# Kernel optimization log

Hardware: AMD Instinct MI355X
Metric: run time of the kernel (lower is better)

## Reference

```python
import jax, jax.numpy as jnp
import numpy as np

B, S, LC, DIM, H, FFN = 1, 3600, 512, 1536, 12, 8960
HD = DIM // H          # 128
GRID = (4, 30, 30)     # f*h*w == S
K_LEN = 9900           # hardcoded k_lens in SelfAttention.forward
EPS = 1e-6

def _rope_axis_angles(n_pos, dim):
    inv = 1.0 / np.power(10000.0, np.arange(0, dim, 2, dtype=np.float64) / dim)
    return np.outer(np.arange(n_pos), inv)

def _build_rope(grid, head_dim):
    c = head_dim // 2                      # 64
    c1, c2 = c - 2 * (c // 3), c // 3      # 22, 21 (Wan 3D rope split)
    f, h, w = grid
    af = _rope_axis_angles(f, 2 * c1)
    ah = _rope_axis_angles(h, 2 * c2)
    aw = _rope_axis_angles(w, 2 * c2)
    ang = np.concatenate([
        np.broadcast_to(af[:, None, None, :], (f, h, w, c1)),
        np.broadcast_to(ah[None, :, None, :], (f, h, w, c2)),
        np.broadcast_to(aw[None, None, :, :], (f, h, w, c2)),
    ], axis=-1).reshape(f * h * w, c)
    return np.cos(ang).astype(np.float32), np.sin(ang).astype(np.float32)

def setup_inputs():
    key = jax.random.key(0)
    ks = iter(jax.random.split(key, 40))
    cos, sin = _build_rope(GRID, HD)
    inp = {
        'x': jax.random.normal(next(ks), (B, S, DIM), dtype=jnp.float32),
        'context': jax.random.normal(next(ks), (B, LC, DIM), dtype=jnp.float32),
        't_mod': 0.1 * jax.random.normal(next(ks), (B, 6, DIM), dtype=jnp.float32),
        'rope_cos': jnp.asarray(cos), 'rope_sin': jnp.asarray(sin),
        'modulation': jax.random.normal(next(ks), (1, 6, DIM), dtype=jnp.float32) / DIM ** 0.5,
    }
    for p in ('sa', 'ca'):
        for w in ('q', 'k', 'v', 'o'):
            inp[p + '_' + w + 'w'] = 0.02 * jax.random.normal(next(ks), (DIM, DIM), dtype=jnp.float32)
            inp[p + '_' + w + 'b'] = jnp.zeros((DIM,), jnp.float32)
        inp[p + '_nq'] = jnp.ones((DIM,), jnp.float32)
        inp[p + '_nk'] = jnp.ones((DIM,), jnp.float32)
    inp['n3_w'] = jnp.ones((DIM,), jnp.float32)
    inp['n3_b'] = jnp.zeros((DIM,), jnp.float32)
    inp['ffn_w1'] = 0.02 * jax.random.normal(next(ks), (DIM, FFN), dtype=jnp.float32)
    inp['ffn_b1'] = jnp.zeros((FFN,), jnp.float32)
    inp['ffn_w2'] = 0.02 * jax.random.normal(next(ks), (FFN, DIM), dtype=jnp.float32)
    inp['ffn_b2'] = jnp.zeros((DIM,), jnp.float32)
    return inp

def _rms(x, w):
    x32 = x.astype(jnp.float32)
    n = x32 * jax.lax.rsqrt(jnp.mean(x32 * x32, axis=-1, keepdims=True) + EPS)
    return n.astype(x.dtype) * w

def _ln(x, w=None, b=None):
    mu = jnp.mean(x, axis=-1, keepdims=True)
    var = jnp.mean(jnp.square(x - mu), axis=-1, keepdims=True)
    y = (x - mu) * jax.lax.rsqrt(var + EPS)
    return y if w is None else y * w + b

def _rope(x, cos, sin):
    b, s, h, d = x.shape
    x2 = x.reshape(b, s, h, d // 2, 2)
    xe, xo = x2[..., 0], x2[..., 1]
    c, sn = cos[None, :, None, :], sin[None, :, None, :]
    return jnp.stack([xe * c - xo * sn, xe * sn + xo * c], axis=-1).reshape(b, s, h, d)

def _attn(q, k, v, k_len=None):
    # q,k,v: [B,S,H,D]
    scores = jnp.einsum('bqhd,bkhd->bhqk', q, k) * (q.shape[-1] ** -0.5)
    if k_len is not None:
        mask = jnp.arange(k.shape[1]) < k_len
        scores = jnp.where(mask[None, None, None, :], scores, jnp.finfo(scores.dtype).min)
    return jnp.einsum('bhqk,bkhd->bqhd', jax.nn.softmax(scores, axis=-1), v)

def reference(x, context, t_mod, rope_cos, rope_sin, modulation,
              sa_qw, sa_qb, sa_kw, sa_kb, sa_vw, sa_vb, sa_ow, sa_ob, sa_nq, sa_nk,
              ca_qw, ca_qb, ca_kw, ca_kb, ca_vw, ca_vb, ca_ow, ca_ob, ca_nq, ca_nk,
              n3_w, n3_b, ffn_w1, ffn_b1, ffn_w2, ffn_b2):
    mod = modulation + t_mod                      # [B,6,DIM]
    sh_msa, sc_msa, g_msa, sh_mlp, sc_mlp, g_mlp = [mod[:, i:i + 1] for i in range(6)]
    b = x.shape[0]
    # --- self-attention with AdaLN modulate + 3D RoPE + k_lens mask ---
    h = _ln(x) * (1 + sc_msa) + sh_msa
    q = _rms(h @ sa_qw + sa_qb, sa_nq).reshape(b, -1, H, HD)
    k = _rms(h @ sa_kw + sa_kb, sa_nk).reshape(b, -1, H, HD)
    v = (h @ sa_vw + sa_vb).reshape(b, -1, H, HD)
    a = _attn(_rope(q, rope_cos, rope_sin), _rope(k, rope_cos, rope_sin), v, k_len=K_LEN)
    x = x + g_msa * (a.reshape(b, -1, DIM) @ sa_ow + sa_ob)
    # --- cross-attention ---
    hc = _ln(x, n3_w, n3_b)
    q = _rms(hc @ ca_qw + ca_qb, ca_nq).reshape(b, -1, H, HD)
    k = _rms(context @ ca_kw + ca_kb, ca_nk).reshape(b, -1, H, HD)
    v = (context @ ca_vw + ca_vb).reshape(b, -1, H, HD)
    x = x + (_attn(q, k, v).reshape(b, -1, DIM) @ ca_ow + ca_ob)
    # --- gated FFN with AdaLN modulate ---
    h = _ln(x) * (1 + sc_mlp) + sh_mlp
    h = jax.nn.gelu(h @ ffn_w1 + ffn_b1, approximate=True) @ ffn_w2 + ffn_b2
    return x + g_mlp * h
```

## Files before the change

kernel.cpp:

```cpp
#include <hip/hip_runtime.h>
#include <cstdint>

#define S_LEN 3600
#define DMODEL 1536
#define LCTX 512
#define NH 12
#define HDIM 128
#define FFND 8960
#define SPAD_SELF 3648

typedef short v8s __attribute__((ext_vector_type(8)));
typedef float v4f __attribute__((ext_vector_type(4)));
typedef unsigned short u16b;
typedef unsigned int u32b;

#define AS1 __attribute__((address_space(1)))
#define AS3 __attribute__((address_space(3)))

__device__ __forceinline__ void gl_lds16(const void* g, void* l){
  __builtin_amdgcn_global_load_lds((AS1 const void*)g, (AS3 void*)l, 16, 0, 0);
}

__device__ __forceinline__ u16b f2b(float f){
  union { float f; u32b i; } x; x.f = f;
  u32b r = x.i + 0x7fffu + ((x.i >> 16) & 1u);
  return (u16b)(r >> 16);
}

__device__ __forceinline__ int swz4(int row){ return (row ^ (row >> 2)) & 3; }

__global__ void add_vec(const float* __restrict__ a, const float* __restrict__ b,
                        float* __restrict__ o, int n){
  int i = blockIdx.x * 256 + threadIdx.x;
  if (i < n) o[i] = a[i] + b[i];
}

__global__ void f2b_kernel(const float* __restrict__ in, u16b* __restrict__ out, int n){
  int i = blockIdx.x * 256 + threadIdx.x;
  if (i < n) out[i] = f2b(in[i]);
}

struct WJob { const float* W; u16b* WT; int K; int N; int t0; };
struct WJobs { WJob j[10]; };

__global__ __launch_bounds__(256) void wconv(WJobs jobs){
  __shared__ float tile[32][33];
  int b = blockIdx.x;
  int ji = 0;
  #pragma unroll
  for (int i = 0; i < 10; ++i) if (b >= jobs.j[i].t0) ji = i;
  WJob jb = jobs.j[ji];
  int rel = b - jb.t0;
  int ntn = jb.N / 32;
  int k0 = (rel / ntn) * 32, n0 = (rel % ntn) * 32;
  int tx = threadIdx.x & 31, ty = threadIdx.x >> 5;
  #pragma unroll
  for (int r = ty; r < 32; r += 8) tile[r][tx] = jb.W[(size_t)(k0 + r) * jb.N + n0 + tx];
  __syncthreads();
  #pragma unroll
  for (int r = ty; r < 32; r += 8) jb.WT[(size_t)(n0 + r) * jb.K + k0 + tx] = f2b(tile[tx][r]);
}

__global__ __launch_bounds__(256) void vtrans(const u16b* __restrict__ V,
                                              u16b* __restrict__ Vt,
                                              int S, int Spad){
  __shared__ u16b t[32][136];
  int h = blockIdx.y, kb = blockIdx.x * 32, tid = threadIdx.x;
  int row = tid >> 3, ch = tid & 7;
  int key = kb + row;
  if (key < S){
    float4 a = *(const float4*)(V + (size_t)key * DMODEL + h * HDIM + ch * 16);
    float4 b = *(const float4*)(V + (size_t)key * DMODEL + h * HDIM + ch * 16 + 8);
    *(float4*)&t[row][ch * 16] = a;
    *(float4*)&t[row][ch * 16 + 8] = b;
  } else {
    float4 z = {0.f, 0.f, 0.f, 0.f};
    *(float4*)&t[row][ch * 16] = z;
    *(float4*)&t[row][ch * 16 + 8] = z;
  }
  __syncthreads();
  int hd = tid >> 1, kc = (tid & 1) * 16;
  u16b* dst = Vt + ((size_t)h * HDIM + hd) * Spad + kb + kc;
  #pragma unroll
  for (int e = 0; e < 16; e += 2){
    u32b pk = ((u32b)t[kc + e][hd]) | (((u32b)t[kc + e + 1][hd]) << 16);
    *(u32b*)(dst + e) = pk;
  }
}

__global__ __launch_bounds__(256) void ln_mod(const float* __restrict__ X,
                                              const float* __restrict__ gamma,
                                              const float* __restrict__ beta,
                                              float gadd, u16b* __restrict__ out){
  int row = blockIdx.x;
  const float* xr = X + (size_t)row * DMODEL;
  int tid = threadIdx.x;
  float v[6]; float s1 = 0.f, s2 = 0.f;
  #pragma unroll
  for (int j = 0; j < 6; ++j){ v[j] = xr[tid + j * 256]; s1 += v[j]; s2 += v[j] * v[j]; }
  #pragma unroll
  for (int o = 1; o < 64; o <<= 1){ s1 += __shfl_xor(s1, o); s2 += __shfl_xor(s2, o); }
  __shared__ float red[8];
  int wid = tid >> 6, lane = tid & 63;
  if (!lane){ red[wid * 2] = s1; red[wid * 2 + 1] = s2; }
  __syncthreads();
  s1 = red[0] + red[2] + red[4] + red[6];
  s2 = red[1] + red[3] + red[5] + red[7];
  float mu = s1 / DMODEL;
  float var = s2 / DMODEL - mu * mu;
  float rstd = rsqrtf(var + 1e-6f);
  #pragma unroll
  for (int j = 0; j < 6; ++j){
    int c = tid + j * 256;
    float g = gamma[c] + gadd;
    float b = beta[c];
    out[(size_t)row * DMODEL + c] = f2b((v[j] - mu) * rstd * g + b);
  }
}

__global__ __launch_bounds__(256) void rms_rope(const float* __restrict__ X,
                                                const float* __restrict__ w,
                                                const float* __restrict__ cosT,
                                                const float* __restrict__ sinT,
                                                u16b* __restrict__ out){
  int row = blockIdx.x;
  const float* xr = X + (size_t)row * DMODEL;
  int tid = threadIdx.x;
  float2 v[3]; float ss = 0.f;
  #pragma unroll
  for (int j = 0; j < 3; ++j){
    v[j] = *(const float2*)(xr + 2 * (tid + j * 256));
    ss += v[j].x * v[j].x + v[j].y * v[j].y;
  }
  #pragma unroll
  for (int o = 1; o < 64; o <<= 1) ss += __shfl_xor(ss, o);
  __shared__ float red[4];
  int wid = tid >> 6, lane = tid & 63;
  if (!lane) red[wid] = ss;
  __syncthreads();
  ss = red[0] + red[1] + red[2] + red[3];
  float rstd = rsqrtf(ss / DMODEL + 1e-6f);
  #pragma unroll
  for (int j = 0; j < 3; ++j){
    int p = tid + j * 256;
    float xe = v[j].x * rstd * w[2 * p];
    float xo = v[j].y * rstd * w[2 * p + 1];
    float oe, oo;
    if (cosT){
      int d = p & 63;
      float c = cosT[row * 64 + d], sn = sinT[row * 64 + d];
      oe = xe * c - xo * sn; oo = xe * sn + xo * c;
    } else { oe = xe; oo = xo; }
    u32b packed = ((u32b)f2b(oe)) | (((u32b)f2b(oo)) << 16);
    *(u32b*)(out + (size_t)row * DMODEL + 2 * p) = packed;
  }
}

template<int EPI>
__global__ __launch_bounds__(256, 2) void gemm_bt(
    const u16b* __restrict__ A, const u16b* __restrict__ BT,
    const float* __restrict__ bias, const float* __restrict__ res,
    const float* __restrict__ gate, float* __restrict__ outF,
    u16b* __restrict__ outB, int M, int N, int K, int kLen)
{
  __shared__ char Asm[2][8192];
  __shared__ char Bsm[2][8192];
  const int tid = threadIdx.x, lane = tid & 63, wid = tid >> 6;
  const int bm = blockIdx.x * 128, bn = blockIdx.y * 128;
  const int kbase = blockIdx.z * kLen;
  const int wm = (wid >> 1) * 64, wn = (wid & 1) * 64;
  v4f acc[4][4] = {};

  auto stage = [&](int buf, int k0){
    #pragma unroll
    for (int c = 0; c < 2; ++c){
      int seg = wid * 2 + c;
      int l = seg * 64 + lane;
      int row = l >> 2, cs = l & 3;
      int col = cs ^ swz4(row);
      gl_lds16(A + (size_t)min(bm + row, M - 1) * K + kbase + k0 + col * 8,
               Asm[buf] + seg * 1024);
      gl_lds16(BT + (size_t)(bn + row) * K + kbase + k0 + col * 8,
               Bsm[buf] + seg * 1024);
    }
  };

  const int nt = kLen / 32;
  int cur = 0;
  stage(0, 0);
  __syncthreads();
  const int chk = lane >> 4, qr = lane & 15;
  for (int t = 0; t < nt; ++t){
    if (t + 1 < nt) stage(cur ^ 1, (t + 1) * 32);
    char* Ab = Asm[cur]; char* Bb = Bsm[cur];
    v8s af[4], bfr[4];
    #pragma unroll
    for (int f = 0; f < 4; ++f){
      int rowa = wm + f * 16 + qr;
      af[f] = *(const v8s*)(Ab + rowa * 64 + ((chk ^ swz4(rowa)) * 16));
      int rowb = wn + f * 16 + qr;
      bfr[f] = *(const v8s*)(Bb + rowb * 64 + ((chk ^ swz4(rowb)) * 16));
    }
    __builtin_amdgcn_s_setprio(1);
    #pragma unroll
    for (int i = 0; i < 4; ++i)
      #pragma unroll
      for (int j = 0; j < 4; ++j)
        acc[i][j] = __builtin_amdgcn_mfma_f32_16x16x32_bf16(af[i], bfr[j], acc[i][j], 0, 0, 0);
    __builtin_amdgcn_s_setprio(0);
    __syncthreads();
    cur ^= 1;
  }
  const int rr = lane >> 4;
  #pragma unroll
  for (int i = 0; i < 4; ++i){
    #pragma unroll
    for (int j = 0; j < 4; ++j){
      int n = bn + wn + j * 16 + qr;
      float bv = (EPI != 5 && bias) ? bias[n] : 0.f;
      float gv = (EPI == 2 && gate) ? gate[n] : 1.f;
      #pragma unroll
      for (int r = 0; r < 4; ++r){
        int m = bm + wm + i * 16 + rr * 4 + r;
        if (m < M){
          float val = acc[i][j][r] + bv;
          size_t idx = (size_t)m * N + n;
          if (EPI == 0) outB[idx] = f2b(val);
          else if (EPI == 1) outF[idx] = val;
          else if (EPI == 2) outF[idx] = res[idx] + gv * val;
          else if (EPI == 5) outF[(size_t)blockIdx.z * M * N + idx] = val;
          else {
            float t3 = val * val * val;
            float th = tanhf(0.7978845608028654f * (val + 0.044715f * t3));
            outB[idx] = f2b(0.5f * val * (1.f + th));
          }
        }
      }
    }
  }
}

struct Seg { const float* bias; float* outF; u16b* outB; };
struct Segs { Seg s[3]; };

__global__ __launch_bounds__(256, 2) void gemm_seg(
    const u16b* __restrict__ A, const u16b* __restrict__ BT,
    Segs segs, int M, int N, int K)
{
  __shared__ char Asm[2][8192];
  __shared__ char Bsm[2][8192];
  const int tid = threadIdx.x, lane = tid & 63, wid = tid >> 6;
  const int bm = blockIdx.x * 128, bn = blockIdx.y * 128;
  const int wm = (wid >> 1) * 64, wn = (wid & 1) * 64;
  v4f acc[4][4] = {};

  auto stage = [&](int buf, int k0){
    #pragma unroll
    for (int c = 0; c < 2; ++c){
      int seg = wid * 2 + c;
      int l = seg * 64 + lane;
      int row = l >> 2, cs = l & 3;
      int col = cs ^ swz4(row);
      gl_lds16(A + (size_t)min(bm + row, M - 1) * K + k0 + col * 8,
               Asm[buf] + seg * 1024);
      gl_lds16(BT + (size_t)(bn + row) * K + k0 + col * 8,
               Bsm[buf] + seg * 1024);
    }
  };

  const int nt = K / 32;
  int cur = 0;
  stage(0, 0);
  __syncthreads();
  const int chk = lane >> 4, qr = lane & 15;
  for (int t = 0; t < nt; ++t){
    if (t + 1 < nt) stage(cur ^ 1, (t + 1) * 32);
    char* Ab = Asm[cur]; char* Bb = Bsm[cur];
    v8s af[4], bfr[4];
    #pragma unroll
    for (int f = 0; f < 4; ++f){
      int rowa = wm + f * 16 + qr;
      af[f] = *(const v8s*)(Ab + rowa * 64 + ((chk ^ swz4(rowa)) * 16));
      int rowb = wn + f * 16 + qr;
      bfr[f] = *(const v8s*)(Bb + rowb * 64 + ((chk ^ swz4(rowb)) * 16));
    }
    __builtin_amdgcn_s_setprio(1);
    #pragma unroll
    for (int i = 0; i < 4; ++i)
      #pragma unroll
      for (int j = 0; j < 4; ++j)
        acc[i][j] = __builtin_amdgcn_mfma_f32_16x16x32_bf16(af[i], bfr[j], acc[i][j], 0, 0, 0);
    __builtin_amdgcn_s_setprio(0);
    __syncthreads();
    cur ^= 1;
  }
  const int seg = bn / 1536;
  const Seg sg = segs.s[seg];
  const int rr = lane >> 4;
  #pragma unroll
  for (int i = 0; i < 4; ++i){
    #pragma unroll
    for (int j = 0; j < 4; ++j){
      int nloc = bn - seg * 1536 + wn + j * 16 + qr;
      float bv = sg.bias[nloc];
      #pragma unroll
      for (int r = 0; r < 4; ++r){
        int m = bm + wm + i * 16 + rr * 4 + r;
        if (m < M){
          float val = acc[i][j][r] + bv;
          size_t idx = (size_t)m * 1536 + nloc;
          if (sg.outB) sg.outB[idx] = f2b(val);
          else sg.outF[idx] = val;
        }
      }
    }
  }
}

__global__ __launch_bounds__(256) void ffn2_reduce(const float* __restrict__ part,
                                                   const float* __restrict__ res,
                                                   const float* __restrict__ bias,
                                                   const float* __restrict__ gate,
                                                   float* __restrict__ out, int total){
  int i4 = blockIdx.x * 256 + threadIdx.x;
  if (i4 * 4 >= total) return;
  int base = i4 * 4;
  int n = base % DMODEL;
  float4 p0 = *(const float4*)(part + base);
  float4 p1 = *(const float4*)(part + (size_t)total + base);
  float4 rs = *(const float4*)(res + base);
  float4 bv = *(const float4*)(bias + n);
  float4 gv = *(const float4*)(gate + n);
  float4 o;
  o.x = rs.x + gv.x * (p0.x + p1.x + bv.x);
  o.y = rs.y + gv.y * (p0.y + p1.y + bv.y);
  o.z = rs.z + gv.z * (p0.z + p1.z + bv.z);
  o.w = rs.w + gv.w * (p0.w + p1.w + bv.w);
  *(float4*)(out + base) = o;
}

__global__ __launch_bounds__(256, 2) void flash_attn(
    const u16b* __restrict__ Q, const u16b* __restrict__ Kp,
    const u16b* __restrict__ Vt, u16b* __restrict__ O,
    int Sq, int Sk, int Spad)
{
  __shared__ char KV[2][32768];
  __shared__ char Pall[8192];
  const int tid = threadIdx.x, lane = tid & 63, wid = tid >> 6;
  const int h = blockIdx.y;
  const int q0 = blockIdx.x * 64 + wid * 16;
  const int qq = lane & 15, cc = lane >> 4;
  char* Pb = Pall + wid * 2048;

  v8s qf[4];
  {
    int qrow = min(q0 + qq, Sq - 1);
    const u16b* qp = Q + (size_t)qrow * DMODEL + h * HDIM + cc * 8;
    #pragma unroll
    for (int ks = 0; ks < 4; ++ks) qf[ks] = *(const v8s*)(qp + ks * 32);
  }

  auto stage = [&](int buf, int kb0){
    char* base = KV[buf];
    #pragma unroll
    for (int c = 0; c < 4; ++c){
      int seg = wid * 4 + c;
      int g = seg * 64 + lane;
      int krow = g >> 4, kcol = (g & 15) ^ (krow & 7);
      gl_lds16(Kp + (size_t)min(kb0 + krow, Sk - 1) * DMODEL + h * HDIM + kcol * 8,
               base + seg * 1024);
      int vrow = g >> 3, vcol = (g & 7) ^ (vrow & 7);
      gl_lds16(Vt + ((size_t)h * HDIM + vrow) * Spad + kb0 + vcol * 8,
               base + 16384 + seg * 1024);
    }
  };

  float mrun = -1e30f, lrun = 0.f;
  v4f oacc[8] = {};
  const float scale = 0.08838834764831845f;
  const int nt = (Sk + 63) >> 6;
  int cur = 0;
  stage(0, 0);
  __syncthreads();

  for (int t = 0; t < nt; ++t){
    if (t + 1 < nt) stage(cur ^ 1, (t + 1) << 6);
    char* Kb = KV[cur]; char* Vb = KV[cur] + 16384;
    int kb0 = t << 6;
    v4f sc[4];
    __builtin_amdgcn_s_setprio(1);
    #pragma unroll
    for (int sub = 0; sub < 4; ++sub){
      v4f sa = {0.f, 0.f, 0.f, 0.f};
      int row = sub * 16 + qq;
      #pragma unroll
      for (int ks = 0; ks < 4; ++ks){
        v8s kf = *(const v8s*)(Kb + row * 256 + (((ks * 4 + cc) ^ (row & 7)) * 16));
        sa = __builtin_amdgcn_mfma_f32_16x16x32_bf16(kf, qf[ks], sa, 0, 0, 0);
      }
      sc[sub] = sa;
    }
    __builtin_amdgcn_s_setprio(0);
    #pragma unroll
    for (int sub = 0; sub < 4; ++sub)
      #pragma unroll
      for (int r = 0; r < 4; ++r) sc[sub][r] *= scale;
    if (kb0 + 64 > Sk){
      #pragma unroll
      for (int sub = 0; sub < 4; ++sub)
        #pragma unroll
        for (int r = 0; r < 4; ++r)
          if (kb0 + sub * 16 + cc * 4 + r >= Sk) sc[sub][r] = -1e30f;
    }
    float pmax = sc[0][0];
    #pragma unroll
    for (int sub = 0; sub < 4; ++sub)
      #pragma unroll
      for (int r = 0; r < 4; ++r) pmax = fmaxf(pmax, sc[sub][r]);
    pmax = fmaxf(pmax, __shfl_xor(pmax, 16));
    pmax = fmaxf(pmax, __shfl_xor(pmax, 32));
    if (!__all(pmax <= mrun + 8.f)){
      float mnew = fmaxf(mrun, pmax);
      float alpha = __expf(mrun - mnew);
      mrun = mnew;
      float alr[4];
      #pragma unroll
      for (int r = 0; r < 4; ++r) alr[r] = __shfl(alpha, cc * 4 + r);
      #pragma unroll
      for (int f = 0; f < 8; ++f)
        #pragma unroll
        for (int r = 0; r < 4; ++r) oacc[f][r] *= alr[r];
      lrun *= alpha;
    }
    float csum = 0.f;
    #pragma unroll
    for (int sub = 0; sub < 4; ++sub)
      #pragma unroll
      for (int r = 0; r < 4; ++r){
        float p = __expf(sc[sub][r] - mrun);
        sc[sub][r] = p; csum += p;
      }
    csum += __shfl_xor(csum, 16);
    csum += __shfl_xor(csum, 32);
    lrun += csum;
    #pragma unroll
    for (int sub = 0; sub < 4; ++sub){
      u32b u01 = ((u32b)f2b(sc[sub][0])) | (((u32b)f2b(sc[sub][1])) << 16);
      u32b u23 = ((u32b)f2b(sc[sub][2])) | (((u32b)f2b(sc[sub][3])) << 16);
      int gI = sub * 2 + (cc >> 1);
      uint2 w2; w2.x = u01; w2.y = u23;
      *(uint2*)(Pb + qq * 128 + ((gI ^ (qq & 7)) * 16) + (cc & 1) * 8) = w2;
    }
    v8s pf0 = *(const v8s*)(Pb + qq * 128 + (((cc) ^ (qq & 7)) * 16));
    v8s pf1 = *(const v8s*)(Pb + qq * 128 + (((4 + cc) ^ (qq & 7)) * 16));
    __builtin_amdgcn_s_setprio(1);
    #pragma unroll
    for (int hdb = 0; hdb < 8; ++hdb){
      int row = hdb * 16 + qq;
      v8s vf0 = *(const v8s*)(Vb + row * 128 + (((cc) ^ (row & 7)) * 16));
      v8s vf1 = *(const v8s*)(Vb + row * 128 + (((4 + cc) ^ (row & 7)) * 16));
      oacc[hdb] = __builtin_amdgcn_mfma_f32_16x16x32_bf16(pf0, vf0, oacc[hdb], 0, 0, 0);
      oacc[hdb] = __builtin_amdgcn_mfma_f32_16x16x32_bf16(pf1, vf1, oacc[hdb], 0, 0, 0);
    }
    __builtin_amdgcn_s_setprio(0);
    __syncthreads();
    cur ^= 1;
  }

  float linv = 1.f / lrun;
  float lr[4];
  #pragma unroll
  for (int r = 0; r < 4; ++r) lr[r] = __shfl(linv, cc * 4 + r);
  #pragma unroll
  for (int hdb = 0; hdb < 8; ++hdb)
    #pragma unroll
    for (int r = 0; r < 4; ++r){
      int qrow = q0 + cc * 4 + r;
      if (qrow < Sq)
        O[(size_t)qrow * DMODEL + h * HDIM + hdb * 16 + qq] = f2b(oacc[hdb][r] * lr[r]);
    }
}

extern "C" void kernel_launch(void* const* d_in, const int* in_sizes, int n_in,
                              void* d_out, int out_size, void* d_ws, size_t ws_size,
                              hipStream_t stream){
  (void)in_sizes; (void)n_in; (void)out_size; (void)ws_size;
  const float* x     = (const float*)d_in[0];
  const float* ctx   = (const float*)d_in[1];
  const float* t_mod = (const float*)d_in[2];
  const float* ropec = (const float*)d_in[3];
  const float* ropes = (const float*)d_in[4];
  const float* modu  = (const float*)d_in[5];
  const float* sa_qw = (const float*)d_in[6];  const float* sa_qb = (const float*)d_in[7];
  const float* sa_kw = (const float*)d_in[8];  const float* sa_kb = (const float*)d_in[9];
  const float* sa_vw = (const float*)d_in[10]; const float* sa_vb = (const float*)d_in[11];
  const float* sa_ow = (const float*)d_in[12]; const float* sa_ob = (const float*)d_in[13];
  const float* sa_nq = (const float*)d_in[14]; const float* sa_nk = (const float*)d_in[15];
  const float* ca_qw = (const float*)d_in[16]; const float* ca_qb = (const float*)d_in[17];
  const float* ca_kw = (const float*)d_in[18]; const float* ca_kb = (const float*)d_in[19];
  const float* ca_vw = (const float*)d_in[20]; const float* ca_vb = (const float*)d_in[21];
  const float* ca_ow = (const float*)d_in[22]; const float* ca_ob = (const float*)d_in[23];
  const float* ca_nq = (const float*)d_in[24]; const float* ca_nk = (const float*)d_in[25];
  const float* n3w   = (const float*)d_in[26]; const float* n3b   = (const float*)d_in[27];
  const float* fw1   = (const float*)d_in[28]; const float* fb1   = (const float*)d_in[29];
  const float* fw2   = (const float*)d_in[30]; const float* fb2   = (const float*)d_in[31];
  float* out = (float*)d_out;

  char* wsp = (char*)d_ws;
  size_t off = 0;
  auto alloc = [&](size_t b){ void* p = wsp + off; off += (b + 255) & ~(size_t)255; return p; };
  const size_t WW = (size_t)DMODEL * DMODEL * 2;
  float* modc = (float*)alloc(6 * DMODEL * 4);
  u16b* w1T   = (u16b*)alloc((size_t)FFND * DMODEL * 2);
  u16b* w2T   = (u16b*)alloc((size_t)DMODEL * FFND * 2);
  u16b* h_bf  = (u16b*)alloc((size_t)S_LEN * DMODEL * 2);
  float* pre0 = (float*)alloc((size_t)S_LEN * DMODEL * 4);
  size_t region0 = off;
  u16b* sa_qkvT = (u16b*)alloc(3 * WW);
  u16b* sa_owT  = (u16b*)alloc(WW);
  u16b* ca_qwT  = (u16b*)alloc(WW);
  u16b* ca_kvT  = (u16b*)alloc(2 * WW);
  u16b* ca_owT  = (u16b*)alloc(WW);
  float* x2    = (float*)alloc((size_t)S_LEN * DMODEL * 4);
  float* pre2  = (float*)alloc((size_t)LCTX * DMODEL * 4);
  u16b* qb     = (u16b*)alloc((size_t)S_LEN * DMODEL * 2);
  u16b* kb     = (u16b*)alloc((size_t)S_LEN * DMODEL * 2);
  u16b* vb     = (u16b*)alloc((size_t)S_LEN * DMODEL * 2);
  u16b* ab     = (u16b*)alloc((size_t)S_LEN * DMODEL * 2);
  u16b* ctxb   = (u16b*)alloc((size_t)LCTX * DMODEL * 2);
  u16b* k2b    = (u16b*)alloc((size_t)LCTX * DMODEL * 2);
  u16b* v2b    = (u16b*)alloc((size_t)LCTX * DMODEL * 2);
  u16b* vts    = (u16b*)alloc((size_t)NH * HDIM * SPAD_SELF * 2);
  u16b* vtc    = (u16b*)alloc((size_t)NH * HDIM * LCTX * 2);
  u16b* fmid = (u16b*)(wsp + region0);
  float* fpart = (float*)(wsp + region0 + (size_t)S_LEN * FFND * 2);

  add_vec<<<36, 256, 0, stream>>>(modu, t_mod, modc, 6 * DMODEL);

  WJobs jobs; int t = 0;
  auto addjob = [&](int i, const float* w_, u16b* wt, int K, int N){
    jobs.j[i].W = w_; jobs.j[i].WT = wt; jobs.j[i].K = K; jobs.j[i].N = N; jobs.j[i].t0 = t;
    t += (K / 32) * (N / 32);
  };
  addjob(0, sa_qw, sa_qkvT, DMODEL, DMODEL);
  addjob(1, sa_kw, sa_qkvT + (size_t)DMODEL * DMODEL, DMODEL, DMODEL);
  addjob(2, sa_vw, sa_qkvT + (size_t)2 * DMODEL * DMODEL, DMODEL, DMODEL);
  addjob(3, sa_ow, sa_owT, DMODEL, DMODEL);
  addjob(4, ca_qw, ca_qwT, DMODEL, DMODEL);
  addjob(5, ca_kw, ca_kvT, DMODEL, DMODEL);
  addjob(6, ca_vw, ca_kvT + (size_t)DMODEL * DMODEL, DMODEL, DMODEL);
  addjob(7, ca_ow, ca_owT, DMODEL, DMODEL);
  addjob(8, fw1, w1T, DMODEL, FFND);
  addjob(9, fw2, w2T, FFND, DMODEL);
  wconv<<<t, 256, 0, stream>>>(jobs);

  f2b_kernel<<<(LCTX * DMODEL) / 256, 256, 0, stream>>>(ctx, ctxb, LCTX * DMODEL);

  ln_mod<<<S_LEN, 256, 0, stream>>>(x, modc + DMODEL, modc, 1.f, h_bf);
  dim3 g12(29, 12);
  {
    Segs sg;
    sg.s[0] = { sa_qb, pre0, nullptr };
    sg.s[1] = { sa_kb, x2,   nullptr };
    sg.s[2] = { sa_vb, nullptr, vb   };
    gemm_seg<<<dim3(29, 36), 256, 0, stream>>>(h_bf, sa_qkvT, sg, S_LEN, 3 * DMODEL, DMODEL);
  }
  rms_rope<<<S_LEN, 256, 0, stream>>>(pre0, sa_nq, ropec, ropes, qb);
  rms_rope<<<S_LEN, 256, 0, stream>>>(x2, sa_nk, ropec, ropes, kb);
  vtrans<<<dim3(SPAD_SELF / 32, 12), 256, 0, stream>>>(vb, vts, S_LEN, SPAD_SELF);
  flash_attn<<<dim3(57, 12), 256, 0, stream>>>(qb, kb, vts, ab, S_LEN, S_LEN, SPAD_SELF);
  gemm_bt<2><<<g12, 256, 0, stream>>>(ab, sa_owT, sa_ob, x, modc + 2 * DMODEL, x2, nullptr, S_LEN, DMODEL, DMODEL, DMODEL);

  ln_mod<<<S_LEN, 256, 0, stream>>>(x2, n3w, n3b, 0.f, h_bf);
  gemm_bt<1><<<g12, 256, 0, stream>>>(h_bf, ca_qwT, ca_qb, nullptr, nullptr, pre0, nullptr, S_LEN, DMODEL, DMODEL, DMODEL);
  {
    Segs sg;
    sg.s[0] = { ca_kb, pre2, nullptr };
    sg.s[1] = { ca_vb, nullptr, v2b  };
    sg.s[2] = { ca_vb, nullptr, v2b  };
    gemm_seg<<<dim3(4, 24), 256, 0, stream>>>(ctxb, ca_kvT, sg, LCTX, 2 * DMODEL, DMODEL);
  }
  rms_rope<<<S_LEN, 256, 0, stream>>>(pre0, ca_nq, nullptr, nullptr, qb);
  rms_rope<<<LCTX, 256, 0, stream>>>(pre2, ca_nk, nullptr, nullptr, k2b);
  vtrans<<<dim3(16, 12), 256, 0, stream>>>(v2b, vtc, LCTX, LCTX);
  flash_attn<<<dim3(57, 12), 256, 0, stream>>>(qb, k2b, vtc, ab, S_LEN, LCTX, LCTX);
  gemm_bt<2><<<g12, 256, 0, stream>>>(ab, ca_owT, ca_ob, x2, nullptr, pre0, nullptr, S_LEN, DMODEL, DMODEL, DMODEL);

  ln_mod<<<S_LEN, 256, 0, stream>>>(pre0, modc + 4 * DMODEL, modc + 3 * DMODEL, 1.f, h_bf);
  gemm_bt<3><<<dim3(29, 70), 256, 0, stream>>>(h_bf, w1T, fb1, nullptr, nullptr, nullptr, fmid, S_LEN, FFND, DMODEL, DMODEL);
  gemm_bt<5><<<dim3(29, 12, 2), 256, 0, stream>>>(fmid, w2T, nullptr, nullptr, nullptr, fpart, nullptr, S_LEN, DMODEL, FFND, FFND / 2);
  ffn2_reduce<<<(S_LEN * DMODEL / 4 + 255) / 256, 256, 0, stream>>>(fpart, pre0, fb2, modc + 5 * DMODEL, out, S_LEN * DMODEL);
}
```

Before: 1.055 ms.

## Split attention over key range with a merge kernel and fold softmax scale into Q

Flash attention now splits the key range into two halves along a third grid dimension. Each half writes unnormalised fp32 partial outputs plus per-row (max, sum) to scratch buffers, and a new merge_o kernel combines them. The aim is more blocks and higher occupancy: the launch bound rises to 4 and the K/V staging drops from double to single buffering. The softmax scale times log2(e) is folded into Q inside rms_rope, so the kernel can use exp2 without a per-score multiply, and P is packed with a native bf16 pack instruction. The cost is an extra kernel, fp32 partial traffic, loss of load/compute overlap within a block, and reuse of existing workspace buffers as scratch; it is not clear the reused kb buffer is large enough to hold fp32 data.

```diff
diff --git a/kernel.cpp b/kernel.cpp
--- a/kernel.cpp
+++ b/kernel.cpp
@@ -25,6 +25,12 @@
   union { float f; u32b i; } x; x.f = f;
   u32b r = x.i + 0x7fffu + ((x.i >> 16) & 1u);
   return (u16b)(r >> 16);
+}
+
+__device__ __forceinline__ u32b cvtpk(float a, float b){
+  u32b r;
+  asm("v_cvt_pk_bf16_f32 %0, %1, %2" : "=v"(r) : "v"(a), "v"(b));
+  return r;
 }
 
 __device__ __forceinline__ int swz4(int row){ return (row ^ (row >> 2)) & 3; }
@@ -122,6 +128,7 @@
                                                 const float* __restrict__ w,
                                                 const float* __restrict__ cosT,
                                                 const float* __restrict__ sinT,
+                                                float qmul,
                                                 u16b* __restrict__ out){
   int row = blockIdx.x;
   const float* xr = X + (size_t)row * DMODEL;
@@ -151,6 +158,7 @@
       float c = cosT[row * 64 + d], sn = sinT[row * 64 + d];
       oe = xe * c - xo * sn; oo = xe * sn + xo * c;
     } else { oe = xe; oo = xo; }
+    oe *= qmul; oo *= qmul;
     u32b packed = ((u32b)f2b(oe)) | (((u32b)f2b(oo)) << 16);
     *(u32b*)(out + (size_t)row * DMODEL + 2 * p) = packed;
   }
@@ -339,17 +347,45 @@
   *(float4*)(out + base) = o;
 }
 
-__global__ __launch_bounds__(256, 2) void flash_attn(
+__global__ __launch_bounds__(256) void merge_o(const float* __restrict__ op0,
+                                               const float* __restrict__ op1,
+                                               const float2* __restrict__ ml,
+                                               u16b* __restrict__ outO, int Sq){
+  int i4 = blockIdx.x * 256 + threadIdx.x;
+  const int perRow = DMODEL / 4;
+  if (i4 >= Sq * perRow) return;
+  int row = i4 / perRow, c4 = (i4 % perRow) * 4;
+  int h = c4 >> 7;
+  float2 ml0 = ml[h * Sq + row];
+  float2 ml1 = ml[NH * Sq + h * Sq + row];
+  float M = fmaxf(ml0.x, ml1.x);
+  float w0 = exp2f(ml0.x - M), w1 = exp2f(ml1.x - M);
+  float inv = 1.f / (ml0.y * w0 + ml1.y * w1);
+  float4 a = *(const float4*)(op0 + (size_t)row * DMODEL + c4);
+  float4 b = *(const float4*)(op1 + (size_t)row * DMODEL + c4);
+  u32b lo = ((u32b)f2b((a.x * w0 + b.x * w1) * inv)) | (((u32b)f2b((a.y * w0 + b.y * w1) * inv)) << 16);
+  u32b hi = ((u32b)f2b((a.z * w0 + b.z * w1) * inv)) | (((u32b)f2b((a.w * w0 + b.w * w1) * inv)) << 16);
+  uint2 w2; w2.x = lo; w2.y = hi;
+  *(uint2*)(outO + (size_t)row * DMODEL + c4) = w2;
+}
+
+__global__ __launch_bounds__(256, 4) void flash_attn(
     const u16b* __restrict__ Q, const u16b* __restrict__ Kp,
     const u16b* __restrict__ Vt, u16b* __restrict__ O,
-    int Sq, int Sk, int Spad)
+    float* __restrict__ op0, float* __restrict__ op1,
+    float2* __restrict__ mlbuf,
+    int Sq, int Sk, int ksplit, int Spad)
 {
-  __shared__ char KV[2][32768];
+  __shared__ char KV[32768];
   __shared__ char Pall[8192];
   const int tid = threadIdx.x, lane = tid & 63, wid = tid >> 6;
   const int h = blockIdx.y;
+  const int z = blockIdx.z;
+  const int kbeg = z * ksplit;
+  const int kend = min(kbeg + ksplit, Sk);
   const int q0 = blockIdx.x * 64 + wid * 16;
   const int qq = lane & 15, cc = lane >> 4;
+  char* Kb = KV; char* Vb = KV + 16384;
   char* Pb = Pall + wid * 2048;
 
   v8s qf[4];
@@ -360,33 +396,28 @@
     for (int ks = 0; ks < 4; ++ks) qf[ks] = *(const v8s*)(qp + ks * 32);
   }
 
-  auto stage = [&](int buf, int kb0){
-    char* base = KV[buf];
+  auto stage = [&](int kb0){
     #pragma unroll
     for (int c = 0; c < 4; ++c){
       int seg = wid * 4 + c;
       int g = seg * 64 + lane;
       int krow = g >> 4, kcol = (g & 15) ^ (krow & 7);
       gl_lds16(Kp + (size_t)min(kb0 + krow, Sk - 1) * DMODEL + h * HDIM + kcol * 8,
-               base + seg * 1024);
+               Kb + seg * 1024);
       int vrow = g >> 3, vcol = (g & 7) ^ (vrow & 7);
       gl_lds16(Vt + ((size_t)h * HDIM + vrow) * Spad + kb0 + vcol * 8,
-               base + 16384 + seg * 1024);
+               Vb + seg * 1024);
     }
   };
 
   float mrun = -1e30f, lrun = 0.f;
   v4f oacc[8] = {};
-  const float scale = 0.08838834764831845f;
-  const int nt = (Sk + 63) >> 6;
-  int cur = 0;
-  stage(0, 0);
-  __syncthreads();
+  const int nt = (kend - kbeg + 63) >> 6;
 
   for (int t = 0; t < nt; ++t){
-    if (t + 1 < nt) stage(cur ^ 1, (t + 1) << 6);
-    char* Kb = KV[cur]; char* Vb = KV[cur] + 16384;
-    int kb0 = t << 6;
+    int kb0 = kbeg + (t << 6);
+    stage(kb0);
+    __syncthreads();
     v4f sc[4];
     __builtin_amdgcn_s_setprio(1);
     #pragma unroll
@@ -401,27 +432,23 @@
       sc[sub] = sa;
     }
     __builtin_amdgcn_s_setprio(0);
-    #pragma unroll
-    for (int sub = 0; sub < 4; ++sub)
-      #pragma unroll
-      for (int r = 0; r < 4; ++r) sc[sub][r] *= scale;
-    if (kb0 + 64 > Sk){
+    if (kb0 + 64 > kend){
       #pragma unroll
       for (int sub = 0; sub < 4; ++sub)
         #pragma unroll
         for (int r = 0; r < 4; ++r)
-          if (kb0 + sub * 16 + cc * 4 + r >= Sk) sc[sub][r] = -1e30f;
-    }
-    float pmax = sc[0][0];
-    #pragma unroll
-    for (int sub = 0; sub < 4; ++sub)
-      #pragma unroll
-      for (int r = 0; r < 4; ++r) pmax = fmaxf(pmax, sc[sub][r]);
+          if (kb0 + sub * 16 + cc * 4 + r >= kend) sc[sub][r] = -1e30f;
+    }
+    float m01 = fmaxf(fmaxf(sc[0][0], sc[0][1]), fmaxf(sc[0][2], sc[0][3]));
+    float m23 = fmaxf(fmaxf(sc[1][0], sc[1][1]), fmaxf(sc[1][2], sc[1][3]));
+    float m45 = fmaxf(fmaxf(sc[2][0], sc[2][1]), fmaxf(sc[2][2], sc[2][3]));
+    float m67 = fmaxf(fmaxf(sc[3][0], sc[3][1]), fmaxf(sc[3][2], sc[3][3]));
+    float pmax = fmaxf(fmaxf(m01, m23), fmaxf(m45, m67));
     pmax = fmaxf(pmax, __shfl_xor(pmax, 16));
     pmax = fmaxf(pmax, __shfl_xor(pmax, 32));
-    if (!__all(pmax <= mrun + 8.f)){
+    if (!__all(pmax <= mrun + 11.54f)){
       float mnew = fmaxf(mrun, pmax);
-      float alpha = __expf(mrun - mnew);
+      float alpha = exp2f(mrun - mnew);
       mrun = mnew;
       float alr[4];
       #pragma unroll
@@ -434,21 +461,26 @@
     }
     float csum = 0.f;
     #pragma unroll
-    for (int sub = 0; sub < 4; ++sub)
-      #pragma unroll
-      for (int r = 0; r < 4; ++r){
-        float p = __expf(sc[sub][r] - mrun);
-        sc[sub][r] = p; csum += p;
+    for (int sub = 0; sub < 4; ++sub){
+      float s0 = 0.f, s1 = 0.f;
+      #pragma unroll
+      for (int r = 0; r < 4; r += 2){
+        float p0 = exp2f(sc[sub][r] - mrun);
+        float p1 = exp2f(sc[sub][r + 1] - mrun);
+        sc[sub][r] = p0; sc[sub][r + 1] = p1;
+        s0 += p0; s1 += p1;
       }
+      csum += s0 + s1;
+    }
     csum += __shfl_xor(csum, 16);
     csum += __shfl_xor(csum, 32);
     lrun += csum;
     #pragma unroll
     for (int sub = 0; sub < 4; ++sub){
-      u32b u01 = ((u32b)f2b(sc[sub][0])) | (((u32b)f2b(sc[sub][1])) << 16);
-      u32b u23 = ((u32b)f2b(sc[sub][2])) | (((u32b)f2b(sc[sub][3])) << 16);
+      uint2 w2;
+      w2.x = cvtpk(sc[sub][0], sc[sub][1]);
+      w2.y = cvtpk(sc[sub][2], sc[sub][3]);
       int gI = sub * 2 + (cc >> 1);
-      uint2 w2; w2.x = u01; w2.y = u23;
       *(uint2*)(Pb + qq * 128 + ((gI ^ (qq & 7)) * 16) + (cc & 1) * 8) = w2;
     }
     v8s pf0 = *(const v8s*)(Pb + qq * 128 + (((cc) ^ (qq & 7)) * 16));
@@ -464,21 +496,34 @@
     }
     __builtin_amdgcn_s_setprio(0);
     __syncthreads();
-    cur ^= 1;
-  }
-
-  float linv = 1.f / lrun;
-  float lr[4];
-  #pragma unroll
-  for (int r = 0; r < 4; ++r) lr[r] = __shfl(linv, cc * 4 + r);
-  #pragma unroll
-  for (int hdb = 0; hdb < 8; ++hdb)
-    #pragma unroll
-    for (int r = 0; r < 4; ++r){
-      int qrow = q0 + cc * 4 + r;
-      if (qrow < Sq)
-        O[(size_t)qrow * DMODEL + h * HDIM + hdb * 16 + qq] = f2b(oacc[hdb][r] * lr[r]);
-    }
+  }
+
+  if (mlbuf){
+    float* op = z ? op1 : op0;
+    #pragma unroll
+    for (int hdb = 0; hdb < 8; ++hdb)
+      #pragma unroll
+      for (int r = 0; r < 4; ++r){
+        int qrow = q0 + cc * 4 + r;
+        if (qrow < Sq)
+          op[(size_t)qrow * DMODEL + h * HDIM + hdb * 16 + qq] = oacc[hdb][r];
+      }
+    if (cc == 0 && q0 + qq < Sq)
+      mlbuf[(size_t)z * NH * Sq + (size_t)h * Sq + q0 + qq] = make_float2(mrun, lrun);
+  } else {
+    float linv = 1.f / lrun;
+    float lr[4];
+    #pragma unroll
+    for (int r = 0; r < 4; ++r) lr[r] = __shfl(linv, cc * 4 + r);
+    #pragma unroll
+    for (int hdb = 0; hdb < 8; ++hdb)
+      #pragma unroll
+      for (int r = 0; r < 4; ++r){
+        int qrow = q0 + cc * 4 + r;
+        if (qrow < Sq)
+          O[(size_t)qrow * DMODEL + h * HDIM + hdb * 16 + qq] = f2b(oacc[hdb][r] * lr[r]);
+      }
+  }
 }
 
 extern "C" void kernel_launch(void* const* d_in, const int* in_sizes, int n_in,
@@ -505,6 +550,8 @@
   const float* fw1   = (const float*)d_in[28]; const float* fb1   = (const float*)d_in[29];
   const float* fw2   = (const float*)d_in[30]; const float* fb2   = (const float*)d_in[31];
   float* out = (float*)d_out;
+
+  const float QSCALE = 0.08838834764831845f * 1.4426950408889634f;
 
   char* wsp = (char*)d_ws;
   size_t off = 0;
@@ -565,10 +612,13 @@
     sg.s[2] = { sa_vb, nullptr, vb   };
     gemm_seg<<<dim3(29, 36), 256, 0, stream>>>(h_bf, sa_qkvT, sg, S_LEN, 3 * DMODEL, DMODEL);
   }
-  rms_rope<<<S_LEN, 256, 0, stream>>>(pre0, sa_nq, ropec, ropes, qb);
-  rms_rope<<<S_LEN, 256, 0, stream>>>(x2, sa_nk, ropec, ropes, kb);
+  rms_rope<<<S_LEN, 256, 0, stream>>>(pre0, sa_nq, ropec, ropes, QSCALE, qb);
+  rms_rope<<<S_LEN, 256, 0, stream>>>(x2, sa_nk, ropec, ropes, 1.f, kb);
   vtrans<<<dim3(SPAD_SELF / 32, 12), 256, 0, stream>>>(vb, vts, S_LEN, SPAD_SELF);
-  flash_attn<<<dim3(57, 12), 256, 0, stream>>>(qb, kb, vts, ab, S_LEN, S_LEN, SPAD_SELF);
+  flash_attn<<<dim3(57, 12, 2), 256, 0, stream>>>(qb, kb, vts, ab,
+      (float*)pre0, (float*)x2, (float2*)vb, S_LEN, S_LEN, 1856, SPAD_SELF);
+  merge_o<<<(S_LEN * (DMODEL / 4) + 255) / 256, 256, 0, stream>>>(
+      (const float*)pre0, (const float*)x2, (const float2*)vb, ab, S_LEN);
   gemm_bt<2><<<g12, 256, 0, stream>>>(ab, sa_owT, sa_ob, x, modc + 2 * DMODEL, x2, nullptr, S_LEN, DMODEL, DMODEL, DMODEL);
 
   ln_mod<<<S_LEN, 256, 0, stream>>>(x2, n3w, n3b, 0.f, h_bf);
@@ -580,10 +630,13 @@
     sg.s[2] = { ca_vb, nullptr, v2b  };
     gemm_seg<<<dim3(4, 24), 256, 0, stream>>>(ctxb, ca_kvT, sg, LCTX, 2 * DMODEL, DMODEL);
   }
-  rms_rope<<<S_LEN, 256, 0, stream>>>(pre0, ca_nq, nullptr, nullptr, qb);
-  rms_rope<<<LCTX, 256, 0, stream>>>(pre2, ca_nk, nullptr, nullptr, k2b);
+  rms_rope<<<S_LEN, 256, 0, stream>>>(pre0, ca_nq, nullptr, nullptr, QSCALE, qb);
+  rms_rope<<<LCTX, 256, 0, stream>>>(pre2, ca_nk, nullptr, nullptr, 1.f, k2b);
   vtrans<<<dim3(16, 12), 256, 0, stream>>>(v2b, vtc, LCTX, LCTX);
-  flash_attn<<<dim3(57, 12), 256, 0, stream>>>(qb, k2b, vtc, ab, S_LEN, LCTX, LCTX);
+  flash_attn<<<dim3(57, 12, 2), 256, 0, stream>>>(qb, k2b, vtc, ab,
+      (float*)pre0, (float*)kb, (float2*)vts, S_LEN, LCTX, 256, LCTX);
+  merge_o<<<(S_LEN * (DMODEL / 4) + 255) / 256, 256, 0, stream>>>(
+      (const float*)pre0, (const float*)kb, (const float2*)vts, ab, S_LEN);
   gemm_bt<2><<<g12, 256, 0, stream>>>(ab, ca_owT, ca_ob, x2, nullptr, pre0, nullptr, S_LEN, DMODEL, DMODEL, DMODEL);
 
   ln_mod<<<S_LEN, 256, 0, stream>>>(pre0, modc + 4 * DMODEL, modc + 3 * DMODEL, 1.f, h_bf);
```

Result: faster. 1.008 ms (-4.5%).
